# Performance work log

Hardware: AMD Instinct MI355X
Metric: run time of the kernel (lower is better)

## Reference

```python
import jax, jax.numpy as jnp
import numpy as np

EPS = 1e-05


def setup_inputs() -> dict:
    key = jax.random.key(0)
    k1, k2, k3 = jax.random.split(key, 3)
    B, T, D = 64, 2048, 768
    outputs = jax.random.normal(k1, (B, T, D), dtype=jnp.float32)
    lens = jax.random.uniform(k2, (B,), dtype=jnp.float32)  # fraction of valid frames
    gnoise_raw = jax.random.normal(k3, (B, D), dtype=jnp.float32)
    return {"outputs": outputs, "lens": lens, "gnoise_raw": gnoise_raw}


def reference(outputs, lens, gnoise_raw):
    # outputs: [B, T, D], lens: [B] (fraction), gnoise_raw: [B, D]
    B, T, D = outputs.shape
    length = lens * T  # float frame counts
    trunc = jnp.floor(length).astype(jnp.int32)  # torch int() truncation (lens > 0)
    count = jnp.clip(trunc + 1, 1, T)            # slice :int(length)+1 -> count frames
    # masked mean over the first `count` frames of each row (single fused pass)
    mask = (jnp.arange(T)[None, :] < count[:, None]).astype(outputs.dtype)  # [B, T]
    masked_mean = jnp.einsum('btd,bt->bd', outputs, mask) / count[:, None].astype(outputs.dtype)
    full_mean = outputs.mean(axis=1)  # used when length == 1
    mean = jnp.where((length != 1.0)[:, None], masked_mean, full_mean)  # [B, D]
    # gaussian noise normalized to [0,1] then scaled: eps*((1-9)*g + 9)
    g = gnoise_raw - jnp.min(gnoise_raw)
    g = g / jnp.max(g)
    gnoise = EPS * ((1.0 - 9.0) * g + 9.0)
    return (mean + gnoise)[:, None, :]  # [B, 1, D]
```

## Files before the change

kernel.cpp:

```cpp
#include <hip/hip_runtime.h>
#include <math.h>

#define B_ 64
#define T_ 2048
#define D_ 768
#define D4_ 192
#define S_ 32
#define EPS_ 1e-5f

static __device__ __forceinline__ int row_count(float lenfrac) {
    float length = lenfrac * (float)T_;
    if (length == 1.0f) return T_;
    int c = (int)floorf(length) + 1;
    if (c < 1) c = 1;
    if (c > T_) c = T_;
    return c;
}

__global__ __launch_bounds__(192) void partial_kernel(const float* __restrict__ outp,
                                                      const float* __restrict__ lens,
                                                      float* __restrict__ partial) {
    const int b = blockIdx.x;
    const int s = blockIdx.y;
    const int tid = threadIdx.x;
    const int tcount = row_count(lens[b]);

    const float4* base = (const float4*)(outp + (size_t)b * (T_ * D_)) + tid;
    float4 a0 = {0.f, 0.f, 0.f, 0.f}, a1 = a0, a2 = a0, a3 = a0;
    int t = s;
    for (; t + 3 * S_ < tcount; t += 4 * S_) {
        float4 v0 = base[(size_t)t * D4_];
        float4 v1 = base[(size_t)(t + S_) * D4_];
        float4 v2 = base[(size_t)(t + 2 * S_) * D4_];
        float4 v3 = base[(size_t)(t + 3 * S_) * D4_];
        a0.x += v0.x; a0.y += v0.y; a0.z += v0.z; a0.w += v0.w;
        a1.x += v1.x; a1.y += v1.y; a1.z += v1.z; a1.w += v1.w;
        a2.x += v2.x; a2.y += v2.y; a2.z += v2.z; a2.w += v2.w;
        a3.x += v3.x; a3.y += v3.y; a3.z += v3.z; a3.w += v3.w;
    }
    for (; t < tcount; t += S_) {
        float4 v0 = base[(size_t)t * D4_];
        a0.x += v0.x; a0.y += v0.y; a0.z += v0.z; a0.w += v0.w;
    }
    float4 acc;
    acc.x = (a0.x + a1.x) + (a2.x + a3.x);
    acc.y = (a0.y + a1.y) + (a2.y + a3.y);
    acc.z = (a0.z + a1.z) + (a2.z + a3.z);
    acc.w = (a0.w + a1.w) + (a2.w + a3.w);

    float4* p = (float4*)partial + ((size_t)s * B_ + b) * D4_ + tid;
    *p = acc;
}

__global__ __launch_bounds__(256) void finalize_kernel(const float* __restrict__ lens,
                                                       const float* __restrict__ graw,
                                                       const float* __restrict__ partial,
                                                       float* __restrict__ outp) {
    const int tid = threadIdx.x;
    const int idx = blockIdx.x * 256 + tid;

    const float4* g4 = (const float4*)graw;
    float vmin = INFINITY, vmax = -INFINITY;
    for (int i = tid; i < B_ * D4_; i += 256) {
        float4 v = g4[i];
        vmin = fminf(vmin, fminf(fminf(v.x, v.y), fminf(v.z, v.w)));
        vmax = fmaxf(vmax, fmaxf(fmaxf(v.x, v.y), fmaxf(v.z, v.w)));
    }
    #pragma unroll
    for (int off = 1; off < 64; off <<= 1) {
        vmin = fminf(vmin, __shfl_xor(vmin, off, 64));
        vmax = fmaxf(vmax, __shfl_xor(vmax, off, 64));
    }
    __shared__ float red[8];
    const int wave = tid >> 6;
    if ((tid & 63) == 0) { red[wave] = vmin; red[4 + wave] = vmax; }
    __syncthreads();
    vmin = fminf(fminf(red[0], red[1]), fminf(red[2], red[3]));
    vmax = fmaxf(fmaxf(red[4], red[5]), fmaxf(red[6], red[7]));
    const float scale = 1.0f / (vmax - vmin);

    const int b = idx / D4_;
    const int c4 = idx - b * D4_;
    const float4* p4 = (const float4*)partial;
    float4 acc = {0.f, 0.f, 0.f, 0.f};
    #pragma unroll
    for (int s = 0; s < S_; ++s) {
        float4 v = p4[((size_t)s * B_ + b) * D4_ + c4];
        acc.x += v.x; acc.y += v.y; acc.z += v.z; acc.w += v.w;
    }
    const float inv = 1.0f / (float)row_count(lens[b]);

    float4 g = g4[idx];
    float4 o;
    o.x = acc.x * inv + EPS_ * (9.0f - 8.0f * ((g.x - vmin) * scale));
    o.y = acc.y * inv + EPS_ * (9.0f - 8.0f * ((g.y - vmin) * scale));
    o.z = acc.z * inv + EPS_ * (9.0f - 8.0f * ((g.z - vmin) * scale));
    o.w = acc.w * inv + EPS_ * (9.0f - 8.0f * ((g.w - vmin) * scale));
    ((float4*)outp)[idx] = o;
}

extern "C" void kernel_launch(void* const* d_in, const int* in_sizes, int n_in,
                              void* d_out, int out_size, void* d_ws, size_t ws_size,
                              hipStream_t stream) {
    const float* outputs = (const float*)d_in[0];
    const float* lens    = (const float*)d_in[1];
    const float* graw    = (const float*)d_in[2];
    float* out = (float*)d_out;
    float* partial = (float*)d_ws;

    partial_kernel<<<dim3(B_, S_), 192, 0, stream>>>(outputs, lens, partial);
    finalize_kernel<<<48, 256, 0, stream>>>(lens, graw, partial, out);
}
```

Measured before the change: 495.7 us.

## Use persistent blocks with atomic work queue over contiguous time chunks

```diff
diff --git a/kernel.cpp b/kernel.cpp
--- a/kernel.cpp
+++ b/kernel.cpp
@@ -5,7 +5,10 @@
 #define T_ 2048
 #define D_ 768
 #define D4_ 192
-#define S_ 32
+#define CHUNK_ 64
+#define NCHUNK_ 32
+#define TASKS_ (B_ * NCHUNK_)
+#define GRID_P_ 1280
 #define EPS_ 1e-5f
 
 static __device__ __forceinline__ int row_count(float lenfrac) {
@@ -17,39 +20,53 @@
     return c;
 }
 
+__global__ void init_kernel(int* __restrict__ counter) {
+    if (threadIdx.x == 0) *counter = GRID_P_;
+}
+
 __global__ __launch_bounds__(192) void partial_kernel(const float* __restrict__ outp,
                                                       const float* __restrict__ lens,
+                                                      int* __restrict__ counter,
                                                       float* __restrict__ partial) {
-    const int b = blockIdx.x;
-    const int s = blockIdx.y;
     const int tid = threadIdx.x;
-    const int tcount = row_count(lens[b]);
+    __shared__ int s_task;
+    int task = blockIdx.x;
+    while (task < TASKS_) {
+        const int b = task & (B_ - 1);
+        const int s = task >> 6;
+        const int tcount = row_count(lens[b]);
+        const int t0 = s * CHUNK_;
+        const int t1 = min(t0 + CHUNK_, tcount);
 
-    const float4* base = (const float4*)(outp + (size_t)b * (T_ * D_)) + tid;
-    float4 a0 = {0.f, 0.f, 0.f, 0.f}, a1 = a0, a2 = a0, a3 = a0;
-    int t = s;
-    for (; t + 3 * S_ < tcount; t += 4 * S_) {
-        float4 v0 = base[(size_t)t * D4_];
-        float4 v1 = base[(size_t)(t + S_) * D4_];
-        float4 v2 = base[(size_t)(t + 2 * S_) * D4_];
-        float4 v3 = base[(size_t)(t + 3 * S_) * D4_];
-        a0.x += v0.x; a0.y += v0.y; a0.z += v0.z; a0.w += v0.w;
-        a1.x += v1.x; a1.y += v1.y; a1.z += v1.z; a1.w += v1.w;
-        a2.x += v2.x; a2.y += v2.y; a2.z += v2.z; a2.w += v2.w;
-        a3.x += v3.x; a3.y += v3.y; a3.z += v3.z; a3.w += v3.w;
+        const float4* base = (const float4*)(outp + (size_t)b * (T_ * D_)) + tid;
+        float4 a0 = {0.f, 0.f, 0.f, 0.f}, a1 = a0, a2 = a0, a3 = a0;
+        int t = t0;
+        for (; t + 3 < t1; t += 4) {
+            float4 v0 = base[(size_t)(t + 0) * D4_];
+            float4 v1 = base[(size_t)(t + 1) * D4_];
+            float4 v2 = base[(size_t)(t + 2) * D4_];
+            float4 v3 = base[(size_t)(t + 3) * D4_];
+            a0.x += v0.x; a0.y += v0.y; a0.z += v0.z; a0.w += v0.w;
+            a1.x += v1.x; a1.y += v1.y; a1.z += v1.z; a1.w += v1.w;
+            a2.x += v2.x; a2.y += v2.y; a2.z += v2.z; a2.w += v2.w;
+            a3.x += v3.x; a3.y += v3.y; a3.z += v3.z; a3.w += v3.w;
+        }
+        for (; t < t1; ++t) {
+            float4 v0 = base[(size_t)t * D4_];
+            a0.x += v0.x; a0.y += v0.y; a0.z += v0.z; a0.w += v0.w;
+        }
+        float4 acc;
+        acc.x = (a0.x + a1.x) + (a2.x + a3.x);
+        acc.y = (a0.y + a1.y) + (a2.y + a3.y);
+        acc.z = (a0.z + a1.z) + (a2.z + a3.z);
+        acc.w = (a0.w + a1.w) + (a2.w + a3.w);
+        ((float4*)partial)[((size_t)s * B_ + b) * D4_ + tid] = acc;
+
+        if (tid == 0) s_task = atomicAdd(counter, 1);
+        __syncthreads();
+        task = s_task;
+        __syncthreads();
     }
-    for (; t < tcount; t += S_) {
-        float4 v0 = base[(size_t)t * D4_];
-        a0.x += v0.x; a0.y += v0.y; a0.z += v0.z; a0.w += v0.w;
-    }
-    float4 acc;
-    acc.x = (a0.x + a1.x) + (a2.x + a3.x);
-    acc.y = (a0.y + a1.y) + (a2.y + a3.y);
-    acc.z = (a0.z + a1.z) + (a2.z + a3.z);
-    acc.w = (a0.w + a1.w) + (a2.w + a3.w);
-
-    float4* p = (float4*)partial + ((size_t)s * B_ + b) * D4_ + tid;
-    *p = acc;
 }
 
 __global__ __launch_bounds__(256) void finalize_kernel(const float* __restrict__ lens,
@@ -84,7 +101,7 @@
     const float4* p4 = (const float4*)partial;
     float4 acc = {0.f, 0.f, 0.f, 0.f};
     #pragma unroll
-    for (int s = 0; s < S_; ++s) {
+    for (int s = 0; s < NCHUNK_; ++s) {
         float4 v = p4[((size_t)s * B_ + b) * D4_ + c4];
         acc.x += v.x; acc.y += v.y; acc.z += v.z; acc.w += v.w;
     }
@@ -106,8 +123,11 @@
     const float* lens    = (const float*)d_in[1];
     const float* graw    = (const float*)d_in[2];
     float* out = (float*)d_out;
-    float* partial = (float*)d_ws;
 
-    partial_kernel<<<dim3(B_, S_), 192, 0, stream>>>(outputs, lens, partial);
+    int*   counter = (int*)d_ws;
+    float* partial = (float*)d_ws + 64;
+
+    init_kernel<<<1, 64, 0, stream>>>(counter);
+    partial_kernel<<<GRID_P_, 192, 0, stream>>>(outputs, lens, counter, partial);
     finalize_kernel<<<48, 256, 0, stream>>>(lens, graw, partial, out);
 }
```

After: 496.2 us. Within noise of the previous version (+0.1%).
